# Kernel tuning notes

Measured on AMD Instinct MI355X. Metric: run time of the kernel, lower is better.

Reference implementation:

```python
import jax, jax.numpy as jnp
import numpy as np

S0, P0 = 4096, 64      # level0 segments, points per level0 segment
S1, P1 = 1024, 256     # level1 superpoints, points per level1 segment
C = 128                # feature dim
KNN = 3                # K (neighbor_range=1 -> 3 candidates)
N = S0 * P0


def setup_inputs() -> dict:
    key = jax.random.key(0)
    ks = jax.random.split(key, 8)
    return {
        "sp_center_feat": jax.random.normal(ks[0], (S1, C), jnp.float32),
        "sp_center_coord": jax.random.normal(ks[1], (S1, 3), jnp.float32),
        "rawPoint_feat": jax.random.normal(ks[2], (N, C), jnp.float32),
        "hilbert_feat_coord": jax.random.normal(ks[3], (N, 3), jnp.float32),
        "points_feat": jax.random.normal(ks[4], (S0, P0, C), jnp.float32),
        "points_coord": jax.random.normal(ks[5], (S0, P0, 3), jnp.float32),
        "level0_to_level1_indices": jnp.sort(jax.random.randint(ks[6], (S0,), 0, S1)).astype(jnp.int64),
        "num_segments0": S0,
        "points_per_segment0": P0,
        "num_segments1": S1,
        "points_per_segment1": P1,
        "K": KNN,
    }


def reference(sp_center_feat, sp_center_coord, rawPoint_feat, hilbert_feat_coord,
              points_feat, points_coord, level0_to_level1_indices,
              num_segments0, points_per_segment0, num_segments1, points_per_segment1, K):
    # --- neighbor superpoint candidates (neighbor_range = 1) ---
    offsets = jnp.arange(-1, 2)                                        # [3]
    nb = jnp.clip(jnp.arange(num_segments0)[:, None] + offsets[None, :], 0, num_segments0 - 1)  # [S0,3]
    sp_idx = level0_to_level1_indices[nb]                              # [S0,3]
    nb_feat = sp_center_feat[sp_idx]                                   # [S0,3,C]
    nb_coord = sp_center_coord[sp_idx]                                 # [S0,3,3]

    # --- cdist + topk (smallest K) ---
    diff = points_coord[:, :, None, :] - nb_coord[:, None, :, :]       # [S0,P0,3,3]
    dist = jnp.sqrt(jnp.maximum(jnp.sum(diff * diff, axis=-1), 0.0))   # [S0,P0,3]
    _, knn_idx = jax.lax.top_k(-dist, K)                               # [S0,P0,K], ascending distance

    # --- gather neighbor feats, dot-product similarity, softmax, argmax ---
    b = jnp.arange(num_segments0)[:, None, None]
    knn_sp_feats = nb_feat[b, knn_idx]                                 # [S0,P0,K,C]
    sim = jnp.einsum('spc,spkc->spk', points_feat, knn_sp_feats)       # [S0,P0,K]
    sim = jax.nn.softmax(sim, axis=-1)
    max_idx = jnp.argmax(sim, axis=-1)                                 # [S0,P0]

    # --- map winning neighbor slot -> superpoint id ---
    sp_knn = sp_idx[b, knn_idx]                                        # [S0,P0,K]
    assigned = jnp.take_along_axis(sp_knn, max_idx[..., None], axis=2)[..., 0]  # [S0,P0]
    point_assignments = assigned.reshape(-1)                           # [N]

    # cross_attention_update_sp is empty -> sp_center_feat passes through unchanged

    # --- scatter-mean: new superpoint centers ---
    seg_sum = jax.ops.segment_sum(hilbert_feat_coord, point_assignments, num_segments=num_segments1)
    counts = jax.ops.segment_sum(jnp.ones((point_assignments.shape[0],), hilbert_feat_coord.dtype),
                                 point_assignments, num_segments=num_segments1)
    new_sp_center_coord = seg_sum / jnp.maximum(counts, 1.0)[:, None]  # [S1,3]

    feat_dim = rawPoint_feat.shape[-1]
    hilbert_feat_level1 = rawPoint_feat.reshape(num_segments1, points_per_segment1, feat_dim)
    points_feat_out = rawPoint_feat.reshape(num_segments0, points_per_segment0, feat_dim)

    return (point_assignments, sp_center_feat, new_sp_center_coord, points_feat_out, hilbert_feat_level1)
```

## Files before the change

### kernel.cpp

```cpp
#include <hip/hip_runtime.h>

#define S0 4096
#define P0 64
#define S1 1024
#define P1 256
#define C  128
#define N_PTS (S0 * P0)

#define SEG_PER_BLK   4
#define PT_PER_BLK    256
#define ASSIGN_BLOCKS (S0 / SEG_PER_BLK)
#define TOTAL_BLOCKS  2048

__global__ __launch_bounds__(256) void fused_kernel(
    const float* __restrict__ sp_feat,
    const float* __restrict__ pts_feat,
    const float* __restrict__ hilb,
    const int*   __restrict__ l01,
    const float4* __restrict__ raw,
    float*  __restrict__ out_assign,
    float4* __restrict__ o_pf,
    float4* __restrict__ o_h1,
    float4* __restrict__ o_spf,
    float*  __restrict__ ws_sum,
    float*  __restrict__ ws_cnt)
{
    __shared__ float cf_lds[6 * C];
    __shared__ float lsum[6][3];
    __shared__ float lcnt[6];
    __shared__ int   lidx[6];

    const int tid = threadIdx.x;
    const int blk = blockIdx.x;

    if (blk < ASSIGN_BLOCKS) {
        const int s_base = blk * SEG_PER_BLK;
        if (tid < 6) {
            int nb = s_base - 1 + tid;
            nb = nb < 0 ? 0 : (nb >= S0 ? S0 - 1 : nb);
            lidx[tid] = l01[nb];
            lcnt[tid] = 0.0f;
        }
        if (tid < 18) lsum[tid / 3][tid % 3] = 0.0f;
        __syncthreads();

        for (int i = tid; i < 6 * C; i += 256)
            cf_lds[i] = sp_feat[(size_t)lidx[i >> 7] * C + (i & (C - 1))];
        __syncthreads();

        const int si  = tid >> 6;
        const int gpt = blk * PT_PER_BLK + tid;
        const float* prow = pts_feat + (size_t)gpt * C;
        const float* c0 = &cf_lds[(si + 0) * C];
        const float* c1 = &cf_lds[(si + 1) * C];
        const float* c2 = &cf_lds[(si + 2) * C];

        float d0 = 0.f, d1 = 0.f, d2 = 0.f;
        #pragma unroll
        for (int j = 0; j < C; j += 4) {
            float4 v  = *reinterpret_cast<const float4*>(prow + j);
            float4 a0 = *reinterpret_cast<const float4*>(c0 + j);
            float4 a1 = *reinterpret_cast<const float4*>(c1 + j);
            float4 a2 = *reinterpret_cast<const float4*>(c2 + j);
            d0 += v.x * a0.x + v.y * a0.y + v.z * a0.z + v.w * a0.w;
            d1 += v.x * a1.x + v.y * a1.y + v.z * a1.z + v.w * a1.w;
            d2 += v.x * a2.x + v.y * a2.y + v.z * a2.z + v.w * a2.w;
        }

        int kb = 0; float best = d0;
        if (d1 > best) { best = d1; kb = 1; }
        if (d2 > best) { best = d2; kb = 2; }
        const int slot = si + kb;

        out_assign[gpt] = (float)lidx[slot];

        atomicAdd(&lsum[slot][0], hilb[(size_t)gpt * 3 + 0]);
        atomicAdd(&lsum[slot][1], hilb[(size_t)gpt * 3 + 1]);
        atomicAdd(&lsum[slot][2], hilb[(size_t)gpt * 3 + 2]);
        atomicAdd(&lcnt[slot], 1.0f);
        __syncthreads();

        if (tid < 6 && lcnt[tid] > 0.0f) {
            atomicAdd(&ws_cnt[lidx[tid]], lcnt[tid]);
            atomicAdd(&ws_sum[(size_t)lidx[tid] * 3 + 0], lsum[tid][0]);
            atomicAdd(&ws_sum[(size_t)lidx[tid] * 3 + 1], lsum[tid][1]);
            atomicAdd(&ws_sum[(size_t)lidx[tid] * 3 + 2], lsum[tid][2]);
        }
    }

    const long NR = (long)N_PTS * C / 4;
    const long NS = (long)S1 * C / 4;
    const long gid    = (long)blk * 256 + tid;
    const long stride = (long)TOTAL_BLOCKS * 256;
    const float4* spf4 = (const float4*)sp_feat;
    for (long i = gid; i < NR; i += stride) {
        float4 v = raw[i];
        o_pf[i] = v;
        o_h1[i] = v;
        if (i < NS) o_spf[i] = spf4[i];
    }
}

__global__ void finalize_kernel(const float* __restrict__ ws_sum,
                                const float* __restrict__ ws_cnt,
                                float* __restrict__ out_coord)
{
    int i = blockIdx.x * blockDim.x + threadIdx.x;
    if (i >= S1 * 3) return;
    out_coord[i] = ws_sum[i] / fmaxf(ws_cnt[i / 3], 1.0f);
}

extern "C" void kernel_launch(void* const* d_in, const int* in_sizes, int n_in,
                              void* d_out, int out_size, void* d_ws, size_t ws_size,
                              hipStream_t stream) {
    const float* sp_feat  = (const float*)d_in[0];
    const float* raw      = (const float*)d_in[2];
    const float* hilb     = (const float*)d_in[3];
    const float* pts_feat = (const float*)d_in[4];
    const int*   l01      = (const int*)d_in[6];

    float* out        = (float*)d_out;
    float* out_assign = out;
    float* out_spfeat = out_assign + N_PTS;
    float* out_coord  = out_spfeat + (size_t)S1 * C;
    float* out_pf     = out_coord + (size_t)S1 * 3;
    float* out_h1     = out_pf + (size_t)S0 * P0 * C;

    float* ws_sum = (float*)d_ws;
    float* ws_cnt = ws_sum + (size_t)S1 * 3;

    hipMemsetAsync(d_ws, 0, (size_t)(S1 * 3 + S1) * sizeof(float), stream);

    fused_kernel<<<TOTAL_BLOCKS, 256, 0, stream>>>(
        sp_feat, pts_feat, hilb, l01, (const float4*)raw,
        out_assign, (float4*)out_pf, (float4*)out_h1, (float4*)out_spfeat,
        ws_sum, ws_cnt);

    finalize_kernel<<<(S1 * 3 + 255) / 256, 256, 0, stream>>>(ws_sum, ws_cnt, out_coord);
}
```

Before: 128.1 us.

## Compute per-point dot products cooperatively with half-wave shuffle reductions

Each wave now owns one segment. A half-wave of 32 lanes reads one point row with coalesced float4 loads, and the three neighbor center vectors sit in registers instead of LDS. The per-lane partial dot products are reduced with xor shuffles, replacing the layout where each thread strided through its own 512-byte row. The intent is to fix the uncoalesced feature reads. The cost is five shuffle steps per row for each of the three candidates, serialized argmax and atomic work on one lane per half-wave, and per-wave partial sums that are flushed to global memory without merging slots that share a superpoint.

```diff
diff --git a/kernel.cpp b/kernel.cpp
--- a/kernel.cpp
+++ b/kernel.cpp
@@ -8,7 +8,6 @@
 #define N_PTS (S0 * P0)
 
 #define SEG_PER_BLK   4
-#define PT_PER_BLK    256
 #define ASSIGN_BLOCKS (S0 / SEG_PER_BLK)
 #define TOTAL_BLOCKS  2048
 
@@ -25,66 +24,76 @@
     float*  __restrict__ ws_sum,
     float*  __restrict__ ws_cnt)
 {
-    __shared__ float cf_lds[6 * C];
-    __shared__ float lsum[6][3];
-    __shared__ float lcnt[6];
-    __shared__ int   lidx[6];
+    __shared__ float lsum[4][3][3];
+    __shared__ float lcnt[4][3];
 
-    const int tid = threadIdx.x;
-    const int blk = blockIdx.x;
+    const int tid  = threadIdx.x;
+    const int blk  = blockIdx.x;
+    const int w    = tid >> 6;
+    const int lane = tid & 63;
 
     if (blk < ASSIGN_BLOCKS) {
-        const int s_base = blk * SEG_PER_BLK;
-        if (tid < 6) {
-            int nb = s_base - 1 + tid;
-            nb = nb < 0 ? 0 : (nb >= S0 ? S0 - 1 : nb);
-            lidx[tid] = l01[nb];
-            lcnt[tid] = 0.0f;
-        }
-        if (tid < 18) lsum[tid / 3][tid % 3] = 0.0f;
+        if (tid < 36) ((float*)lsum)[tid] = 0.0f;
+        if (tid < 12) ((float*)lcnt)[tid] = 0.0f;
         __syncthreads();
 
-        for (int i = tid; i < 6 * C; i += 256)
-            cf_lds[i] = sp_feat[(size_t)lidx[i >> 7] * C + (i & (C - 1))];
+        const int s  = blk * SEG_PER_BLK + w;
+        const int sm = (s - 1 < 0) ? 0 : s - 1;
+        const int sp = (s + 1 >= S0) ? S0 - 1 : s + 1;
+        const int id0 = l01[sm], id1 = l01[s], id2 = l01[sp];
+
+        const int h = lane >> 5;
+        const int q = (lane & 31) * 4;
+
+        const float4 c0 = *reinterpret_cast<const float4*>(sp_feat + (size_t)id0 * C + q);
+        const float4 c1 = *reinterpret_cast<const float4*>(sp_feat + (size_t)id1 * C + q);
+        const float4 c2 = *reinterpret_cast<const float4*>(sp_feat + (size_t)id2 * C + q);
+
+        const float* segb = pts_feat + (size_t)s * P0 * C;
+
+        #pragma unroll 4
+        for (int k = 0; k < 32; ++k) {
+            const int row = 2 * k + h;
+            float4 v = *reinterpret_cast<const float4*>(segb + (size_t)row * C + q);
+            float p0 = v.x * c0.x + v.y * c0.y + v.z * c0.z + v.w * c0.w;
+            float p1 = v.x * c1.x + v.y * c1.y + v.z * c1.z + v.w * c1.w;
+            float p2 = v.x * c2.x + v.y * c2.y + v.z * c2.z + v.w * c2.w;
+            #pragma unroll
+            for (int off = 1; off < 32; off <<= 1) {
+                p0 += __shfl_xor(p0, off);
+                p1 += __shfl_xor(p1, off);
+                p2 += __shfl_xor(p2, off);
+            }
+            if ((lane & 31) == 0) {
+                int kb = 0; float best = p0;
+                if (p1 > best) { best = p1; kb = 1; }
+                if (p2 > best) { best = p2; kb = 2; }
+                const int gpt = s * P0 + row;
+                out_assign[gpt] = (float)(kb == 0 ? id0 : (kb == 1 ? id1 : id2));
+                const float* hp = hilb + (size_t)gpt * 3;
+                atomicAdd(&lsum[w][kb][0], hp[0]);
+                atomicAdd(&lsum[w][kb][1], hp[1]);
+                atomicAdd(&lsum[w][kb][2], hp[2]);
+                atomicAdd(&lcnt[w][kb], 1.0f);
+            }
+        }
         __syncthreads();
 
-        const int si  = tid >> 6;
-        const int gpt = blk * PT_PER_BLK + tid;
-        const float* prow = pts_feat + (size_t)gpt * C;
-        const float* c0 = &cf_lds[(si + 0) * C];
-        const float* c1 = &cf_lds[(si + 1) * C];
-        const float* c2 = &cf_lds[(si + 2) * C];
-
-        float d0 = 0.f, d1 = 0.f, d2 = 0.f;
-        #pragma unroll
-        for (int j = 0; j < C; j += 4) {
-            float4 v  = *reinterpret_cast<const float4*>(prow + j);
-            float4 a0 = *reinterpret_cast<const float4*>(c0 + j);
-            float4 a1 = *reinterpret_cast<const float4*>(c1 + j);
-            float4 a2 = *reinterpret_cast<const float4*>(c2 + j);
-            d0 += v.x * a0.x + v.y * a0.y + v.z * a0.z + v.w * a0.w;
-            d1 += v.x * a1.x + v.y * a1.y + v.z * a1.z + v.w * a1.w;
-            d2 += v.x * a2.x + v.y * a2.y + v.z * a2.z + v.w * a2.w;
+        if (tid < 12) {
+            const int ww = tid >> 2;
         }
-
-        int kb = 0; float best = d0;
-        if (d1 > best) { best = d1; kb = 1; }
-        if (d2 > best) { best = d2; kb = 2; }
-        const int slot = si + kb;
-
-        out_assign[gpt] = (float)lidx[slot];
-
-        atomicAdd(&lsum[slot][0], hilb[(size_t)gpt * 3 + 0]);
-        atomicAdd(&lsum[slot][1], hilb[(size_t)gpt * 3 + 1]);
-        atomicAdd(&lsum[slot][2], hilb[(size_t)gpt * 3 + 2]);
-        atomicAdd(&lcnt[slot], 1.0f);
-        __syncthreads();
-
-        if (tid < 6 && lcnt[tid] > 0.0f) {
-            atomicAdd(&ws_cnt[lidx[tid]], lcnt[tid]);
-            atomicAdd(&ws_sum[(size_t)lidx[tid] * 3 + 0], lsum[tid][0]);
-            atomicAdd(&ws_sum[(size_t)lidx[tid] * 3 + 1], lsum[tid][1]);
-            atomicAdd(&ws_sum[(size_t)lidx[tid] * 3 + 2], lsum[tid][2]);
+        if (tid < 12) {
+            const int ww = tid / 3, kb = tid % 3;
+            if (lcnt[ww][kb] > 0.0f) {
+                const int s2 = blk * SEG_PER_BLK + ww;
+                int nb = s2 - 1 + kb;
+                nb = nb < 0 ? 0 : (nb >= S0 ? S0 - 1 : nb);
+                const int id = l01[nb];
+                atomicAdd(&ws_cnt[id], lcnt[ww][kb]);
+                atomicAdd(&ws_sum[(size_t)id * 3 + 0], lsum[ww][kb][0]);
+                atomicAdd(&ws_sum[(size_t)id * 3 + 1], lsum[ww][kb][1]);
+                atomicAdd(&ws_sum[(size_t)id * 3 + 2], lsum[ww][kb][2]);
+            }
         }
     }
 
```

Measured after the change: 127.2 us. Within noise of the previous version (-0.7%).
